# Optimization experiments

Measured on AMD Instinct MI355X. Metric: run time of the kernel, lower is better.

Reference implementation:

```python
import jax, jax.numpy as jnp
import numpy as np

N_NODES = 50000
N_EDGES = 800000
IN_CH = 64
HID = 128
LAST_HID = 256


def setup_inputs() -> dict:
    key = jax.random.key(0)
    ks = jax.random.split(key, 12)
    x = jax.random.normal(ks[0], (N_NODES, IN_CH), dtype=jnp.float32)
    edge_index = jax.random.randint(ks[1], (2, N_EDGES), 0, N_NODES, dtype=jnp.int64)
    s = lambda fan_in: 1.0 / np.sqrt(fan_in)
    return {
        "x": x,
        "edge_index": edge_index,
        # SAGEConv1: lin_l (aggregated neighbors, with bias), lin_r (root, no bias)
        "W1l": jax.random.normal(ks[2], (HID, IN_CH), dtype=jnp.float32) * s(IN_CH),
        "b1l": jnp.zeros((HID,), dtype=jnp.float32),
        "W1r": jax.random.normal(ks[3], (HID, IN_CH), dtype=jnp.float32) * s(IN_CH),
        # SAGEConv2 -> 1 channel
        "W2l": jax.random.normal(ks[4], (1, HID), dtype=jnp.float32) * s(HID),
        "b2l": jnp.zeros((1,), dtype=jnp.float32),
        "W2r": jax.random.normal(ks[5], (1, HID), dtype=jnp.float32) * s(HID),
        # fc1 (LazyLinear bound to N_NODES input features) and fc2
        "fc1_W": jax.random.normal(ks[6], (LAST_HID, N_NODES), dtype=jnp.float32) * s(N_NODES),
        "fc1_b": jnp.zeros((LAST_HID,), dtype=jnp.float32),
        "fc2_W": jax.random.normal(ks[7], (1, LAST_HID), dtype=jnp.float32) * s(LAST_HID),
        "fc2_b": jnp.zeros((1,), dtype=jnp.float32),
    }


def _sage_conv(h, src, dst, Wl, bl, Wr, n_nodes):
    # PyG SAGEConv (mean aggr): out = lin_l(mean_{j in N(i)} x_j) + lin_r(x_i)
    msgs = h[src]  # [E, F] gather of source node features
    summed = jax.ops.segment_sum(msgs, dst, num_segments=n_nodes)  # [N, F]
    deg = jax.ops.segment_sum(jnp.ones((src.shape[0],), h.dtype), dst, num_segments=n_nodes)
    agg = summed / jnp.maximum(deg, 1.0)[:, None]
    return agg @ Wl.T + bl + h @ Wr.T


def reference(x, edge_index, W1l, b1l, W1r, W2l, b2l, W2r, fc1_W, fc1_b, fc2_W, fc2_b):
    n = x.shape[0]
    src, dst = edge_index[0], edge_index[1]
    h = jax.nn.relu(_sage_conv(x, src, dst, W1l, b1l, W1r, n))   # [N, HID]
    h = jax.nn.relu(_sage_conv(h, src, dst, W2l, b2l, W2r, n))   # [N, 1]
    v = h[:, 0]                                                   # [N]
    z = fc1_W @ v + fc1_b                                         # [LAST_HID]
    pred = fc2_W @ z + fc2_b                                      # [1]
    return pred[0]  # scalar (torch.squeeze)
```

## Files before the change

### kernel.cpp

```cpp
#include <hip/hip_runtime.h>

#define N_NODESC 50000
#define N_EDGESC 800000
#define MAXDEG 64

typedef short bf16x8 __attribute__((ext_vector_type(8)));
typedef float f32x4  __attribute__((ext_vector_type(4)));

__device__ inline unsigned short f2bf(float f) {
    unsigned u = __float_as_uint(f);
    unsigned r = u + 0x7FFFu + ((u >> 16) & 1u);
    return (unsigned short)(r >> 16);
}
__device__ inline float bf2f(unsigned short h) {
    return __uint_as_float(((unsigned)h) << 16);
}

__global__ void k0_init(int* __restrict__ deg, float* __restrict__ z) {
    int i = blockIdx.x * 256 + threadIdx.x;
    if (i < N_NODESC) deg[i] = 0;
    if (i < 256) z[i] = 0.0f;
}

#define K1_BLOCKS 2048
#define K1_EPB (N_EDGESC / (K1_BLOCKS / 8))
__global__ void k1_bucket(const int* __restrict__ ei, int* __restrict__ deg,
                          int* __restrict__ bucket) {
    int g   = blockIdx.x & 7;
    int idx = blockIdx.x >> 3;
    int lo = g * (N_NODESC / 8), hi = lo + (N_NODESC / 8);
    int e0 = idx * K1_EPB;
    for (int i = threadIdx.x; i < K1_EPB; i += 256) {
        int e = e0 + i;
        int dst = ei[N_EDGESC + e];
        int src = ei[e];
        if (dst >= lo && dst < hi) {
            int slot = atomicAdd(&deg[dst], 1);
            if (slot < MAXDEG) bucket[dst * MAXDEG + slot] = src;
        }
    }
}

__global__ void k2_agg(const float* __restrict__ x, const int* __restrict__ deg,
                       const int* __restrict__ bucket, float* __restrict__ agg) {
    int lane = threadIdx.x & 63;
    int node = blockIdx.x * 4 + (threadIdx.x >> 6);
    int g  = lane >> 4;
    int c4 = lane & 15;
    int d = deg[node];
    int c = min(d, MAXDEG);
    int bidx = bucket[node * MAXDEG + lane];
    float4 acc = make_float4(0.f, 0.f, 0.f, 0.f);
    for (int k = 0; k < c; k += 8) {
        int i0 = k + g, i1 = k + 4 + g;
        int b0 = __shfl(bidx, i0);
        int b1 = __shfl(bidx, i1);
        if (i0 < c) {
            float4 v = ((const float4*)(x + b0 * 64))[c4];
            acc.x += v.x; acc.y += v.y; acc.z += v.z; acc.w += v.w;
        }
        if (i1 < c) {
            float4 v = ((const float4*)(x + b1 * 64))[c4];
            acc.x += v.x; acc.y += v.y; acc.z += v.z; acc.w += v.w;
        }
    }
    #pragma unroll
    for (int m = 16; m <= 32; m <<= 1) {
        acc.x += __shfl_xor(acc.x, m);
        acc.y += __shfl_xor(acc.y, m);
        acc.z += __shfl_xor(acc.z, m);
        acc.w += __shfl_xor(acc.w, m);
    }
    if (g == 0) {
        float inv = 1.0f / (float)max(d, 1);
        ((float4*)(agg + node * 64))[c4] =
            make_float4(acc.x * inv, acc.y * inv, acc.z * inv, acc.w * inv);
    }
}

#define K3S 144

__launch_bounds__(256, 3)
__global__ void k3_mm_mfma(const float* __restrict__ x, const float* __restrict__ agg,
                           const float* __restrict__ W1l, const float* __restrict__ b1l,
                           const float* __restrict__ W1r,
                           const float* __restrict__ W2l, const float* __restrict__ W2r,
                           float* __restrict__ s_out, float* __restrict__ t_out) {
    __shared__ __align__(16) short sAhi[64 * K3S];
    __shared__ __align__(16) short sAlo[64 * K3S];
    __shared__ float sS[64], sT[64];

    int tid = threadIdx.x;
    int lane = tid & 63;
    int wave = tid >> 6;
    int col = lane & 15;
    int quad = lane >> 4;
    int node0 = blockIdx.x * 64;

    if (tid < 64) { sS[tid] = 0.f; sT[tid] = 0.f; }

    int o_base = wave * 32;
    bf16x8 bhi[2][4], blo[2][4];
    float bias_r[2], w2l_r[2], w2r_r[2];
    #pragma unroll
    for (int oc = 0; oc < 2; oc++) {
        int o = o_base + oc * 16 + col;
        bias_r[oc] = b1l[o]; w2l_r[oc] = W2l[o]; w2r_r[oc] = W2r[o];
        #pragma unroll
        for (int ks = 0; ks < 4; ks++) {
            int k0 = ks * 32 + quad * 8;
            const float* wrow = (k0 < 64) ? (W1r + o * 64 + k0)
                                          : (W1l + o * 64 + (k0 - 64));
            #pragma unroll
            for (int j = 0; j < 8; j++) {
                float w = wrow[j];
                unsigned short h = f2bf(w);
                bhi[oc][ks][j] = (short)h;
                blo[oc][ks][j] = (short)f2bf(w - bf2f(h));
            }
        }
    }

    #pragma unroll
    for (int i = 0; i < 4; i++) {
        int c = tid + 256 * i;
        int n = c >> 4, kc = c & 15;
        int node = node0 + n;
        float v[8];
        if (node < N_NODESC) {
            const float* src = (kc < 8) ? (x + node * 64 + kc * 8)
                                        : (agg + node * 64 + (kc - 8) * 8);
            float4 v0 = *(const float4*)src;
            float4 v1 = *(const float4*)(src + 4);
            v[0] = v0.x; v[1] = v0.y; v[2] = v0.z; v[3] = v0.w;
            v[4] = v1.x; v[5] = v1.y; v[6] = v1.z; v[7] = v1.w;
        } else {
            #pragma unroll
            for (int j = 0; j < 8; j++) v[j] = 0.f;
        }
        bf16x8 hv, lv;
        #pragma unroll
        for (int j = 0; j < 8; j++) {
            unsigned short h = f2bf(v[j]);
            hv[j] = (short)h;
            lv[j] = (short)f2bf(v[j] - bf2f(h));
        }
        *(bf16x8*)&sAhi[n * K3S + kc * 8] = hv;
        *(bf16x8*)&sAlo[n * K3S + kc * 8] = lv;
    }
    __syncthreads();

    f32x4 acc[4][2];
    #pragma unroll
    for (int nt = 0; nt < 4; nt++)
        #pragma unroll
        for (int oc = 0; oc < 2; oc++) acc[nt][oc] = (f32x4)0.f;

    #pragma unroll
    for (int ks = 0; ks < 4; ks++) {
        #pragma unroll
        for (int nt = 0; nt < 4; nt++) {
            int off = (nt * 16 + col) * K3S + ks * 32 + quad * 8;
            bf16x8 ah = *(const bf16x8*)&sAhi[off];
            bf16x8 al = *(const bf16x8*)&sAlo[off];
            #pragma unroll
            for (int oc = 0; oc < 2; oc++) {
                acc[nt][oc] = __builtin_amdgcn_mfma_f32_16x16x32_bf16(ah, bhi[oc][ks], acc[nt][oc], 0, 0, 0);
                acc[nt][oc] = __builtin_amdgcn_mfma_f32_16x16x32_bf16(al, bhi[oc][ks], acc[nt][oc], 0, 0, 0);
                acc[nt][oc] = __builtin_amdgcn_mfma_f32_16x16x32_bf16(ah, blo[oc][ks], acc[nt][oc], 0, 0, 0);
            }
        }
    }

    #pragma unroll
    for (int nt = 0; nt < 4; nt++) {
        float sp[4] = {0.f, 0.f, 0.f, 0.f};
        float tp[4] = {0.f, 0.f, 0.f, 0.f};
        #pragma unroll
        for (int oc = 0; oc < 2; oc++)
            #pragma unroll
            for (int reg = 0; reg < 4; reg++) {
                float h = fmaxf(acc[nt][oc][reg] + bias_r[oc], 0.f);
                sp[reg] += h * w2l_r[oc];
                tp[reg] += h * w2r_r[oc];
            }
        #pragma unroll
        for (int reg = 0; reg < 4; reg++) {
            #pragma unroll
            for (int m = 1; m <= 8; m <<= 1) {
                sp[reg] += __shfl_xor(sp[reg], m);
                tp[reg] += __shfl_xor(tp[reg], m);
            }
        }
        if (col == 0) {
            int nn = nt * 16 + quad * 4;
            #pragma unroll
            for (int reg = 0; reg < 4; reg++) {
                atomicAdd(&sS[nn + reg], sp[reg]);
                atomicAdd(&sT[nn + reg], tp[reg]);
            }
        }
    }
    __syncthreads();
    if (tid < 64) {
        int node = node0 + tid;
        if (node < N_NODESC) { s_out[node] = sS[tid]; t_out[node] = sT[tid]; }
    }
}

__global__ void k4_layer2(const float* __restrict__ s, const float* __restrict__ t,
                          const int* __restrict__ deg, const int* __restrict__ bucket,
                          const float* __restrict__ b2l, float* __restrict__ v) {
    int tid = threadIdx.x;
    int lane = tid & 15;
    int node = blockIdx.x * 16 + (tid >> 4);
    int d = deg[node];
    int c = min(d, MAXDEG);
    float sum = 0.f;
    for (int k = lane; k < c; k += 16) sum += s[bucket[node * MAXDEG + k]];
    sum += __shfl_xor(sum, 1);
    sum += __shfl_xor(sum, 2);
    sum += __shfl_xor(sum, 4);
    sum += __shfl_xor(sum, 8);
    if (lane == 0) {
        float h = sum / (float)max(d, 1) + b2l[0] + t[node];
        v[node] = fmaxf(h, 0.f);
    }
}

__global__ void k5_fc1(const float* __restrict__ fc1W, const float* __restrict__ v,
                       float* __restrict__ z) {
    int row = blockIdx.x >> 2;
    int part = blockIdx.x & 3;
    const float4* W4 = (const float4*)(fc1W + row * 50000 + part * 12500);
    const float4* v4 = (const float4*)(v + part * 12500);
    float sum = 0.f;
    for (int i = threadIdx.x; i < 3125; i += 256) {
        float4 w = W4[i], a = v4[i];
        sum += w.x * a.x + w.y * a.y + w.z * a.z + w.w * a.w;
    }
    #pragma unroll
    for (int m = 1; m < 64; m <<= 1) sum += __shfl_xor(sum, m);
    __shared__ float red[4];
    if ((threadIdx.x & 63) == 0) red[threadIdx.x >> 6] = sum;
    __syncthreads();
    if (threadIdx.x == 0) atomicAdd(&z[row], red[0] + red[1] + red[2] + red[3]);
}

__global__ void k6_head(const float* __restrict__ z, const float* __restrict__ fc1b,
                        const float* __restrict__ fc2W, const float* __restrict__ fc2b,
                        float* __restrict__ out) {
    int t = threadIdx.x;
    float val = (z[t] + fc1b[t]) * fc2W[t];
    #pragma unroll
    for (int m = 1; m < 64; m <<= 1) val += __shfl_xor(val, m);
    __shared__ float red[4];
    if ((t & 63) == 0) red[t >> 6] = val;
    __syncthreads();
    if (t == 0) out[0] = red[0] + red[1] + red[2] + red[3] + fc2b[0];
}

extern "C" void kernel_launch(void* const* d_in, const int* in_sizes, int n_in,
                              void* d_out, int out_size, void* d_ws, size_t ws_size,
                              hipStream_t stream) {
    const float* x    = (const float*)d_in[0];
    const int*   ei   = (const int*)d_in[1];
    const float* W1l  = (const float*)d_in[2];
    const float* b1l  = (const float*)d_in[3];
    const float* W1r  = (const float*)d_in[4];
    const float* W2l  = (const float*)d_in[5];
    const float* b2l  = (const float*)d_in[6];
    const float* W2r  = (const float*)d_in[7];
    const float* fc1W = (const float*)d_in[8];
    const float* fc1b = (const float*)d_in[9];
    const float* fc2W = (const float*)d_in[10];
    const float* fc2b = (const float*)d_in[11];
    float* out = (float*)d_out;

    char* ws = (char*)d_ws;
    int*   deg    = (int*)  (ws + 0);
    float* z      = (float*)(ws + 200192);
    int*   bucket = (int*)  (ws + 201216);
    float* agg    = (float*)(ws + 13001216);
    float* s      = (float*)(ws + 25801216);
    float* t      = (float*)(ws + 26001216);
    float* v      = (float*)(ws + 26201216);

    k0_init   <<<196,   256, 0, stream>>>(deg, z);
    k1_bucket <<<K1_BLOCKS, 256, 0, stream>>>(ei, deg, bucket);
    k2_agg    <<<12500, 256, 0, stream>>>(x, deg, bucket, agg);
    k3_mm_mfma<<<782,  256, 0, stream>>>(x, agg, W1l, b1l, W1r, W2l, W2r, s, t);
    k4_layer2 <<<3125,  256, 0, stream>>>(s, t, deg, bucket, b2l, v);
    k5_fc1    <<<1024,  256, 0, stream>>>(fc1W, v, z);
    k6_head   <<<1,     256, 0, stream>>>(z, fc1b, fc2W, fc2b, out);
}
```

Before: 214.6 us.

## Bucket edges by 16-node groups with packed dst and fp16 feature gather

Replaces the per-node fixed-slot bucket with per-group buckets of 16 destination nodes that hold the source index and local dst packed into one int. This cuts atomic contention and bucket footprint. The aggregation kernel counting-sorts each group's edges in shared memory and then gathers fp16-converted features, roughly halving gather bytes. Layer 2 accumulates with shared-memory atomics per group. Risks are fp16 precision loss in the aggregation, src packed into 16 bits (node ids up to 50000 fit), a new conversion kernel pass, and dropped edges if a group exceeds 512.

```diff
diff --git a/kernel.cpp b/kernel.cpp
--- a/kernel.cpp
+++ b/kernel.cpp
@@ -1,8 +1,10 @@
 #include <hip/hip_runtime.h>
+#include <hip/hip_fp16.h>
 
 #define N_NODESC 50000
 #define N_EDGESC 800000
-#define MAXDEG 64
+#define N_GROUPS 3125
+#define GSLOTS 512
 
 typedef short bf16x8 __attribute__((ext_vector_type(8)));
 typedef float f32x4  __attribute__((ext_vector_type(4)));
@@ -16,16 +18,27 @@
     return __uint_as_float(((unsigned)h) << 16);
 }
 
-__global__ void k0_init(int* __restrict__ deg, float* __restrict__ z) {
+__global__ void k0_init(int* __restrict__ gcnt, float* __restrict__ z) {
     int i = blockIdx.x * 256 + threadIdx.x;
-    if (i < N_NODESC) deg[i] = 0;
+    if (i < N_GROUPS) gcnt[i] = 0;
     if (i < 256) z[i] = 0.0f;
+}
+
+__global__ void k_half(const float* __restrict__ x, __half* __restrict__ xh) {
+    int i = (blockIdx.x * 256 + threadIdx.x) * 4;
+    float4 f = *(const float4*)(x + i);
+    __half2 h01 = __floats2half2_rn(f.x, f.y);
+    __half2 h23 = __floats2half2_rn(f.z, f.w);
+    uint2 u;
+    u.x = *(unsigned*)&h01;
+    u.y = *(unsigned*)&h23;
+    *(uint2*)(xh + i) = u;
 }
 
 #define K1_BLOCKS 2048
 #define K1_EPB (N_EDGESC / (K1_BLOCKS / 8))
-__global__ void k1_bucket(const int* __restrict__ ei, int* __restrict__ deg,
-                          int* __restrict__ bucket) {
+__global__ void k1_bucket(const int* __restrict__ ei, int* __restrict__ gcnt,
+                          int* __restrict__ gbucket) {
     int g   = blockIdx.x & 7;
     int idx = blockIdx.x >> 3;
     int lo = g * (N_NODESC / 8), hi = lo + (N_NODESC / 8);
@@ -33,48 +46,72 @@
     for (int i = threadIdx.x; i < K1_EPB; i += 256) {
         int e = e0 + i;
         int dst = ei[N_EDGESC + e];
-        int src = ei[e];
         if (dst >= lo && dst < hi) {
-            int slot = atomicAdd(&deg[dst], 1);
-            if (slot < MAXDEG) bucket[dst * MAXDEG + slot] = src;
-        }
-    }
-}
-
-__global__ void k2_agg(const float* __restrict__ x, const int* __restrict__ deg,
-                       const int* __restrict__ bucket, float* __restrict__ agg) {
-    int lane = threadIdx.x & 63;
-    int node = blockIdx.x * 4 + (threadIdx.x >> 6);
-    int g  = lane >> 4;
-    int c4 = lane & 15;
-    int d = deg[node];
-    int c = min(d, MAXDEG);
-    int bidx = bucket[node * MAXDEG + lane];
-    float4 acc = make_float4(0.f, 0.f, 0.f, 0.f);
-    for (int k = 0; k < c; k += 8) {
-        int i0 = k + g, i1 = k + 4 + g;
-        int b0 = __shfl(bidx, i0);
-        int b1 = __shfl(bidx, i1);
-        if (i0 < c) {
-            float4 v = ((const float4*)(x + b0 * 64))[c4];
-            acc.x += v.x; acc.y += v.y; acc.z += v.z; acc.w += v.w;
-        }
-        if (i1 < c) {
-            float4 v = ((const float4*)(x + b1 * 64))[c4];
-            acc.x += v.x; acc.y += v.y; acc.z += v.z; acc.w += v.w;
-        }
-    }
-    #pragma unroll
-    for (int m = 16; m <= 32; m <<= 1) {
-        acc.x += __shfl_xor(acc.x, m);
-        acc.y += __shfl_xor(acc.y, m);
-        acc.z += __shfl_xor(acc.z, m);
-        acc.w += __shfl_xor(acc.w, m);
-    }
-    if (g == 0) {
-        float inv = 1.0f / (float)max(d, 1);
-        ((float4*)(agg + node * 64))[c4] =
-            make_float4(acc.x * inv, acc.y * inv, acc.z * inv, acc.w * inv);
+            int src = ei[e];
+            int grp = dst >> 4;
+            int slot = atomicAdd(&gcnt[grp], 1);
+            if (slot < GSLOTS) gbucket[grp * GSLOTS + slot] = src | ((dst & 15) << 16);
+        }
+    }
+}
+
+__global__ void k2_agg(const __half* __restrict__ xh, const int* __restrict__ gcnt,
+                       const int* __restrict__ gbucket, float* __restrict__ agg) {
+    __shared__ int eArr[GSLOTS];
+    __shared__ unsigned short sorted[GSLOTS];
+    __shared__ int hist[16], offs[17], cursor[16];
+
+    int g = blockIdx.x;
+    int tid = threadIdx.x;
+    int cnt = min(gcnt[g], GSLOTS);
+
+    if (tid < 16) hist[tid] = 0;
+    __syncthreads();
+    for (int i = tid; i < cnt; i += 256) {
+        int p = gbucket[g * GSLOTS + i];
+        eArr[i] = p;
+        atomicAdd(&hist[(p >> 16) & 15], 1);
+    }
+    __syncthreads();
+    if (tid == 0) {
+        int r = 0;
+        #pragma unroll
+        for (int j = 0; j < 16; j++) { offs[j] = r; r += hist[j]; }
+        offs[16] = r;
+    }
+    __syncthreads();
+    if (tid < 16) cursor[tid] = offs[tid];
+    __syncthreads();
+    for (int i = tid; i < cnt; i += 256) {
+        int p = eArr[i];
+        int pos = atomicAdd(&cursor[(p >> 16) & 15], 1);
+        sorted[pos] = (unsigned short)(p & 0xFFFF);
+    }
+    __syncthreads();
+
+    int lane = tid & 63;
+    int w = tid >> 6;
+    int hsel = lane >> 5;
+    int c2 = lane & 31;
+
+    #pragma unroll
+    for (int ni = 0; ni < 4; ni++) {
+        int n = w * 4 + ni;
+        int b = offs[n], e = offs[n + 1];
+        float ax = 0.f, ay = 0.f;
+        for (int j = b + hsel; j < e; j += 2) {
+            int src = sorted[j];
+            __half2 h = *(const __half2*)(xh + src * 64 + c2 * 2);
+            float2 f = __half22float2(h);
+            ax += f.x; ay += f.y;
+        }
+        ax += __shfl_xor(ax, 32);
+        ay += __shfl_xor(ay, 32);
+        if (lane < 32) {
+            int node = g * 16 + n;
+            float inv = 1.0f / (float)max(e - b, 1);
+            *(float2*)(agg + node * 64 + c2 * 2) = make_float2(ax * inv, ay * inv);
+        }
     }
 }
 
@@ -209,21 +246,24 @@
 }
 
 __global__ void k4_layer2(const float* __restrict__ s, const float* __restrict__ t,
-                          const int* __restrict__ deg, const int* __restrict__ bucket,
+                          const int* __restrict__ gcnt, const int* __restrict__ gbucket,
                           const float* __restrict__ b2l, float* __restrict__ v) {
-    int tid = threadIdx.x;
-    int lane = tid & 15;
-    int node = blockIdx.x * 16 + (tid >> 4);
-    int d = deg[node];
-    int c = min(d, MAXDEG);
-    float sum = 0.f;
-    for (int k = lane; k < c; k += 16) sum += s[bucket[node * MAXDEG + k]];
-    sum += __shfl_xor(sum, 1);
-    sum += __shfl_xor(sum, 2);
-    sum += __shfl_xor(sum, 4);
-    sum += __shfl_xor(sum, 8);
-    if (lane == 0) {
-        float h = sum / (float)max(d, 1) + b2l[0] + t[node];
+    __shared__ float accS[16];
+    __shared__ int cntS[16];
+    int g = blockIdx.x;
+    int lane = threadIdx.x;
+    if (lane < 16) { accS[lane] = 0.f; cntS[lane] = 0; }
+    __syncthreads();
+    int cnt = min(gcnt[g], GSLOTS);
+    for (int i = lane; i < cnt; i += 64) {
+        int p = gbucket[g * GSLOTS + i];
+        atomicAdd(&accS[(p >> 16) & 15], s[p & 0xFFFF]);
+        atomicAdd(&cntS[(p >> 16) & 15], 1);
+    }
+    __syncthreads();
+    if (lane < 16) {
+        int node = g * 16 + lane;
+        float h = accS[lane] / (float)max(cntS[lane], 1) + b2l[0] + t[node];
         v[node] = fmaxf(h, 0.f);
     }
 }
@@ -277,20 +317,22 @@
     const float* fc2b = (const float*)d_in[11];
     float* out = (float*)d_out;
 
-    char* ws = (char*)d_ws;
-    int*   deg    = (int*)  (ws + 0);
-    float* z      = (float*)(ws + 200192);
-    int*   bucket = (int*)  (ws + 201216);
-    float* agg    = (float*)(ws + 13001216);
-    float* s      = (float*)(ws + 25801216);
-    float* t      = (float*)(ws + 26001216);
-    float* v      = (float*)(ws + 26201216);
-
-    k0_init   <<<196,   256, 0, stream>>>(deg, z);
-    k1_bucket <<<K1_BLOCKS, 256, 0, stream>>>(ei, deg, bucket);
-    k2_agg    <<<12500, 256, 0, stream>>>(x, deg, bucket, agg);
-    k3_mm_mfma<<<782,  256, 0, stream>>>(x, agg, W1l, b1l, W1r, W2l, W2r, s, t);
-    k4_layer2 <<<3125,  256, 0, stream>>>(s, t, deg, bucket, b2l, v);
-    k5_fc1    <<<1024,  256, 0, stream>>>(fc1W, v, z);
-    k6_head   <<<1,     256, 0, stream>>>(z, fc1b, fc2W, fc2b, out);
-}
+    char*   ws      = (char*)d_ws;
+    int*    gcnt    = (int*)   (ws + 0);
+    float*  z       = (float*) (ws + 12800);
+    __half* xh      = (__half*)(ws + 14336);
+    int*    gbucket = (int*)   (ws + 6414336);
+    float*  agg     = (float*) (ws + 12814336);
+    float*  s       = (float*) (ws + 25614336);
+    float*  t       = (float*) (ws + 25814336);
+    float*  v       = (float*) (ws + 26014336);
+
+    k0_init   <<<16,        256, 0, stream>>>(gcnt, z);
+    k_half    <<<3125,      256, 0, stream>>>(x, xh);
+    k1_bucket <<<K1_BLOCKS, 256, 0, stream>>>(ei, gcnt, gbucket);
+    k2_agg    <<<N_GROUPS,  256, 0, stream>>>(xh, gcnt, gbucket, agg);
+    k3_mm_mfma<<<782,       256, 0, stream>>>(x, agg, W1l, b1l, W1r, W2l, W2r, s, t);
+    k4_layer2 <<<N_GROUPS,   64, 0, stream>>>(s, t, gcnt, gbucket, b2l, v);
+    k5_fc1    <<<1024,      256, 0, stream>>>(fc1W, v, z);
+    k6_head   <<<1,         256, 0, stream>>>(z, fc1b, fc2W, fc2b, out);
+}
```

Result: slower. 313.0 us (+45.9%).
